# Kernel tuning notes

Measured on AMD Instinct MI355X. Metric: run time of the kernel, lower is better.

Reference implementation:

```python
import jax, jax.numpy as jnp
import numpy as np

NUM_NODE = 50000
NUM_EDGE = 1_600_000
NUM_REL = 512
DIM = 64


def setup_inputs() -> dict:
    key = jax.random.key(0)
    k1, k2, k3, k4, k5, k6 = jax.random.split(key, 6)
    inp = jax.random.normal(k1, (NUM_NODE, DIM), dtype=jnp.float32)
    boundary = jax.random.normal(k2, (NUM_NODE, DIM), dtype=jnp.float32)
    node_in = jax.random.randint(k3, (NUM_EDGE,), 0, NUM_NODE)
    node_out = jax.random.randint(k4, (NUM_EDGE,), 0, NUM_NODE)
    rel = jax.random.randint(k5, (NUM_EDGE,), 0, NUM_REL)
    edge_list = jnp.stack([node_in, node_out, rel], axis=1).astype(jnp.int32)
    edge_weight = jnp.ones((NUM_EDGE,), dtype=jnp.float32)
    relation_weight = jax.random.normal(k6, (NUM_REL, DIM), dtype=jnp.float32)
    W = jax.random.normal(jax.random.fold_in(key, 7), (DIM, DIM), dtype=jnp.float32) / np.sqrt(DIM)
    b = jnp.zeros((DIM,), dtype=jnp.float32)
    return {"input": inp, "boundary": boundary, "edge_list": edge_list,
            "edge_weight": edge_weight, "relation_weight": relation_weight,
            "W": W, "b": b}


def reference(input, boundary, edge_list, edge_weight, relation_weight, W, b):
    node_in = edge_list[:, 0]
    node_out = edge_list[:, 1]
    rel = edge_list[:, 2]
    # message: DistMult = x_src * r_e   [E, D]
    msg = input[node_in] * relation_weight[rel]
    msg = msg * edge_weight[:, None]
    # std aggregation: sum and sq_sum scatters, boundary acts as an extra self-message
    s = jax.ops.segment_sum(msg, node_out, num_segments=NUM_NODE) + boundary
    sq = jax.ops.segment_sum(msg * msg, node_out, num_segments=NUM_NODE) + boundary * boundary
    deg = jax.ops.segment_sum(jnp.ones_like(edge_weight), node_out, num_segments=NUM_NODE)
    deg1 = (deg + 1.0)[:, None]  # degree_out + 1 (boundary counted)
    update = jnp.sqrt(jnp.clip(sq / deg1 - (s / deg1) ** 2, 1e-6))
    # add_model: single Linear (MLP with num_mlp_layer=1, no trailing activation)
    return update @ W.T + b
```

## Files before the change

kernel.cpp:

```cpp
#include <hip/hip_runtime.h>
#include <hip/hip_bf16.h>
#include <hip/hip_fp16.h>

#define NN  50000
#define NE  1600000
#define DIM 64
#define NBK 391

#define OFF_FLAGS  0
#define OFF_BOFF   8
#define OFF_BCNTP  400
#define OFF_BCURP  8000
#define OFF_INP16  50800
#define OFF_RELW16 1650800
#define OFF_EIDX_H 1667184

#define CHUNK 4096
#define SBCAP 7936

typedef __bf16 bf16x8 __attribute__((ext_vector_type(8)));
typedef __bf16 bf16x4 __attribute__((ext_vector_type(4)));
typedef float  f32x4  __attribute__((ext_vector_type(4)));

__device__ __forceinline__ float loadF(const void* p, int i, int bf) {
  if (bf) return __bfloat162float(((const __hip_bfloat16*)p)[i]);
  return ((const float*)p)[i];
}

__device__ __forceinline__ float4 loadF4(const void* p, int i4, int bf) {
  if (bf) {
    ushort4 u = ((const ushort4*)p)[i4];
    float4 f;
    union { unsigned int ui; float fl; } c;
    c.ui = (unsigned int)u.x << 16; f.x = c.fl;
    c.ui = (unsigned int)u.y << 16; f.y = c.fl;
    c.ui = (unsigned int)u.z << 16; f.z = c.fl;
    c.ui = (unsigned int)u.w << 16; f.w = c.fl;
    return f;
  }
  return ((const float4*)p)[i4];
}

__device__ __forceinline__ float4 h4f(ushort4 u) {
  float4 f;
  f.x = __half2float(__ushort_as_half(u.x));
  f.y = __half2float(__ushort_as_half(u.y));
  f.z = __half2float(__ushort_as_half(u.z));
  f.w = __half2float(__ushort_as_half(u.w));
  return f;
}

__device__ __forceinline__ void accum(ushort4 ua, ushort4 ur,
                                      float4& s4, float4& q4) {
  float4 a = h4f(ua), r = h4f(ur);
  float tx = a.x * r.x, ty = a.y * r.y, tz = a.z * r.z, tw = a.w * r.w;
  s4.x += tx; q4.x = fmaf(tx, tx, q4.x);
  s4.y += ty; q4.y = fmaf(ty, ty, q4.y);
  s4.z += tz; q4.z = fmaf(tz, tz, q4.z);
  s4.w += tw; q4.w = fmaf(tw, tw, q4.w);
}

__global__ void k_detect(const void* input, const void* boundary,
                         const void* relw, const void* W, const void* ew,
                         int* flags, int* bcntp) {
  __shared__ int cnt;
  int t = threadIdx.x;
  const void* arrs[4] = {input, boundary, relw, W};
  for (int a = 0; a < 4; ++a) {
    if (t == 0) cnt = 0;
    __syncthreads();
    const unsigned short* u = (const unsigned short*)arrs[a];
    unsigned ex = (u[2 * t] >> 7) & 0xFF;
    if (ex >= 100 && ex <= 140) atomicAdd(&cnt, 1);
    __syncthreads();
    if (t == 0) flags[a] = (cnt >= 32) ? 1 : 0;
    __syncthreads();
  }
  if (t == 0) {
    flags[4] = (((const unsigned short*)ew)[0] == 0x3F80) ? 1 : 0;
    flags[5] = 1;
  }
  for (int i = t; i < NBK * 16; i += 64) bcntp[i] = 0;
}

__global__ __launch_bounds__(256) void k_stage(const void* __restrict__ in,
                                               const void* __restrict__ rw,
                                               unsigned short* __restrict__ inph,
                                               unsigned short* __restrict__ rwh,
                                               const int* __restrict__ flags) {
  if (flags[0] || flags[2]) return;
  int i = blockIdx.x * 256 + threadIdx.x;
  if (i < NN * 16) {
    float4 v = ((const float4*)in)[i];
    ushort4 h;
    h.x = __half_as_ushort(__float2half(v.x));
    h.y = __half_as_ushort(__float2half(v.y));
    h.z = __half_as_ushort(__float2half(v.z));
    h.w = __half_as_ushort(__float2half(v.w));
    ((ushort4*)inph)[i] = h;
  }
  if (i < 512 * 16) {
    float4 v = ((const float4*)rw)[i];
    ushort4 h;
    h.x = __half_as_ushort(__float2half(v.x));
    h.y = __half_as_ushort(__float2half(v.y));
    h.z = __half_as_ushort(__float2half(v.z));
    h.w = __half_as_ushort(__float2half(v.w));
    ((ushort4*)rwh)[i] = h;
  }
}

__global__ __launch_bounds__(256) void k_bhist(const int* __restrict__ el,
                                               const void* __restrict__ ew,
                                               int* __restrict__ bcntp,
                                               int* __restrict__ flags) {
  __shared__ int lc[NBK];
  int t = threadIdx.x;
  int bfE = flags[4];
  for (int i = t; i < NBK; i += 256) lc[i] = 0;
  __syncthreads();
  int c0 = blockIdx.x * 8192;
  int bad = 0;
  for (int i = t; i < 8192; i += 256) {
    int e = c0 + i;
    if (e < NE) {
      atomicAdd(&lc[el[e * 3 + 1] >> 7], 1);
      if (loadF(ew, e, bfE) != 1.0f) bad = 1;
    }
  }
  if (bad) flags[5] = 0;
  __syncthreads();
  for (int i = t; i < NBK; i += 256)
    if (lc[i]) atomicAdd(&bcntp[i * 16], lc[i]);
}

__global__ __launch_bounds__(256) void k_scanb(const int* __restrict__ bcntp,
                                               int* __restrict__ boff,
                                               int* __restrict__ bcurp) {
  __shared__ int sc[256];
  int t = threadIdx.x;
  int i0 = 2 * t, i1 = 2 * t + 1;
  int a = (i0 < NBK) ? bcntp[i0 * 16] : 0;
  int b = (i1 < NBK) ? bcntp[i1 * 16] : 0;
  sc[t] = a + b;
  __syncthreads();
  for (int off = 1; off < 256; off <<= 1) {
    int v = (t >= off) ? sc[t - off] : 0;
    __syncthreads();
    sc[t] += v;
    __syncthreads();
  }
  int excl = sc[t] - (a + b);
  if (i0 < 392) boff[i0] = excl;
  if (i1 < 392) boff[i1] = excl + a;
  if (i0 < NBK) bcurp[i0 * 16] = excl;
  if (i1 < NBK) bcurp[i1 * 16] = excl + a;
}

__global__ __launch_bounds__(256) void k_parta(
    const int* __restrict__ el, int* __restrict__ bcurp,
    int* __restrict__ eidx, const int* __restrict__ flags,
    const int* __restrict__ boff, int gb0, int gb1, int cap) {
  __shared__ int stage[CHUNK];
  __shared__ unsigned short sbk[CHUNK];
  __shared__ int lh[NBK], lbase[NBK], lh2[NBK], gbs[NBK];
  __shared__ int sc[256];
  __shared__ int total;
  int t = threadIdx.x;
  int nb = gb1 - gb0;
  int c0 = blockIdx.x * CHUNK;
  int ones = flags[5];
  int base0 = boff[gb0];
  for (int i = t; i < nb; i += 256) { lh[i] = 0; lh2[i] = 0; }
  __syncthreads();
  for (int i = t; i < CHUNK; i += 256) {
    int e = c0 + i;
    if (e < NE) {
      int b = (el[e * 3 + 1] >> 7) - gb0;
      if (b >= 0 && b < nb) atomicAdd(&lh[b], 1);
    }
  }
  __syncthreads();
  int a0 = (2 * t < nb) ? lh[2 * t] : 0;
  int a1 = (2 * t + 1 < nb) ? lh[2 * t + 1] : 0;
  sc[t] = a0 + a1;
  __syncthreads();
  for (int off = 1; off < 256; off <<= 1) {
    int v = (t >= off) ? sc[t - off] : 0;
    __syncthreads();
    sc[t] += v;
    __syncthreads();
  }
  int excl = sc[t] - (a0 + a1);
  if (2 * t < nb) {
    lbase[2 * t] = excl;
    if (a0 > 0) gbs[2 * t] = atomicAdd(&bcurp[(gb0 + 2 * t) * 16], a0);
  }
  if (2 * t + 1 < nb) {
    lbase[2 * t + 1] = excl + a0;
    if (a1 > 0) gbs[2 * t + 1] = atomicAdd(&bcurp[(gb0 + 2 * t + 1) * 16], a1);
  }
  if (t == 255) total = sc[255];
  __syncthreads();
  for (int i = t; i < CHUNK; i += 256) {
    int e = c0 + i;
    if (e < NE) {
      int nout = el[e * 3 + 1];
      int b = (nout >> 7) - gb0;
      if (b >= 0 && b < nb) {
        int r = atomicAdd(&lh2[b], 1);
        int slot = lbase[b] + r;
        int rec = ones ? (el[e * 3] | (el[e * 3 + 2] << 16) |
                          ((nout & 127) << 25))
                       : (e | ((nout & 127) << 25));
        stage[slot] = rec;
        sbk[slot] = (unsigned short)b;
      }
    }
  }
  __syncthreads();
  int tot = total;
  for (int i = t; i < tot; i += 256) {
    int b = sbk[i];
    int dst = gbs[b] + (i - lbase[b]) - base0;
    if (dst >= 0 && dst < cap) eidx[dst] = stage[i];
  }
}

__global__ __launch_bounds__(1024, 8) void k_node(
    const void* __restrict__ input, const void* __restrict__ boundary,
    const int* __restrict__ el, const void* __restrict__ ew,
    const void* __restrict__ relw, const void* __restrict__ W,
    const void* __restrict__ bv, const int* __restrict__ boff,
    const int* __restrict__ eidx, const int* __restrict__ flags,
    const unsigned short* __restrict__ inph,
    const unsigned short* __restrict__ rwh,
    void* __restrict__ out, int gb0, int hi, int cap) {
  __shared__ int ld[SBCAP];
  __shared__ int ld2[SBCAP];
  __shared__ int lstart[128], lend[128], lcnt[128];
  __bf16 (*updb)[72] = reinterpret_cast<__bf16(*)[72]>(ld);

  int bfI = flags[0], bfB = flags[1], bfR = flags[2], bfW = flags[3],
      bfE = flags[4], ones = flags[5];
  int t = threadIdx.x;
  int wv = t >> 6, ln = t & 63;
  int g = ln >> 4;
  int k = ln & 15;
  int q = ln >> 4;
  int B = gb0 + blockIdx.x;
  int n0 = B * 128;
  int base0 = boff[gb0];
  int rbase = boff[B], rend = boff[B + 1];
  int cnt = rend - rbase;
  int fast = (cnt <= SBCAP) && (rend - base0 <= cap);

  if (t < 128) lcnt[t] = 0;
  __syncthreads();
  if (fast) {
    for (int i = t; i < cnt; i += 1024) ld[i] = eidx[rbase - base0 + i];
    __syncthreads();
    for (int i = t; i < cnt; i += 1024)
      atomicAdd(&lcnt[(((unsigned)ld[i]) >> 25) & 127], 1);
  }
  __syncthreads();
  if (t < 128) lend[t] = lcnt[t];
  __syncthreads();
  for (int off = 1; off < 128; off <<= 1) {
    int v = 0;
    if (t < 128 && t >= off) v = lend[t - off];
    __syncthreads();
    if (t < 128) lend[t] += v;
    __syncthreads();
  }
  if (t < 128) { lstart[t] = lend[t] - lcnt[t]; lcnt[t] = 0; }
  __syncthreads();
  if (fast) {
    for (int i = t; i < cnt; i += 1024) {
      int rec = ld[i];
      int l = (((unsigned)rec) >> 25) & 127;
      int r = atomicAdd(&lcnt[l], 1);
      ld2[lstart[l] + r] = rec;
    }
  }
  __syncthreads();

  const ushort4* ih4 = (const ushort4*)inph;
  const ushort4* rh4 = (const ushort4*)rwh;
  int hot = (!bfI && !bfR && ones && inph != 0) ? 1 : 0;

  for (int rr = 0; rr < 8; ++rr) {
    int row = wv * 8 + rr;
    int n = n0 + row;
    if (n >= hi) {
      if (g == 0) *(bf16x4*)&updb[row][4 * k] =
          bf16x4{(__bf16)0.f, (__bf16)0.f, (__bf16)0.f, (__bf16)0.f};
      continue;
    }
    float4 s4 = {0.f,0.f,0.f,0.f}, q4 = {0.f,0.f,0.f,0.f};
    float degf = 0.f;
    if (fast) {
      int start = lstart[row], end = lend[row];
      degf = (float)(end - start);
      if (hot) {
        for (int base = start; base < end; base += 64) {
          int mm = end - base; if (mm > 64) mm = 64;
          int rec = 0;
          if (ln < mm) rec = ld2[base + ln];
          int jq = mm >> 2;
          int jmax = (mm + 3) >> 2;
          int j = 0;
          for (; j + 4 <= jq; j += 4) {
            int pk0 = __shfl(rec, j * 4 + g);
            int pk1 = __shfl(rec, j * 4 + 4 + g);
            int pk2 = __shfl(rec, j * 4 + 8 + g);
            int pk3 = __shfl(rec, j * 4 + 12 + g);
            ushort4 a0 = ih4[(pk0 & 0xFFFF) * 16 + k];
            ushort4 r0 = rh4[((pk0 >> 16) & 0x1FF) * 16 + k];
            ushort4 a1 = ih4[(pk1 & 0xFFFF) * 16 + k];
            ushort4 r1 = rh4[((pk1 >> 16) & 0x1FF) * 16 + k];
            ushort4 a2 = ih4[(pk2 & 0xFFFF) * 16 + k];
            ushort4 r2 = rh4[((pk2 >> 16) & 0x1FF) * 16 + k];
            ushort4 a3 = ih4[(pk3 & 0xFFFF) * 16 + k];
            ushort4 r3 = rh4[((pk3 >> 16) & 0x1FF) * 16 + k];
            accum(a0, r0, s4, q4);
            accum(a1, r1, s4, q4);
            accum(a2, r2, s4, q4);
            accum(a3, r3, s4, q4);
          }
          for (; j < jq; ++j) {
            int pk = __shfl(rec, j * 4 + g);
            ushort4 a = ih4[(pk & 0xFFFF) * 16 + k];
            ushort4 r = rh4[((pk >> 16) & 0x1FF) * 16 + k];
            accum(a, r, s4, q4);
          }
          for (; j < jmax; ++j) {
            int slot = j * 4 + g;
            int pk = __shfl(rec, slot & 63);
            float wsel = (slot < mm) ? 1.0f : 0.0f;
            ushort4 ua = ih4[(pk & 0xFFFF) * 16 + k];
            ushort4 ur = rh4[((pk >> 16) & 0x1FF) * 16 + k];
            float4 a = h4f(ua), r = h4f(ur);
            float tx = a.x*r.x, ty = a.y*r.y, tz = a.z*r.z, tw = a.w*r.w;
            s4.x = fmaf(wsel, tx, s4.x); q4.x = fmaf(wsel*tx, tx, q4.x);
            s4.y = fmaf(wsel, ty, s4.y); q4.y = fmaf(wsel*ty, ty, q4.y);
            s4.z = fmaf(wsel, tz, s4.z); q4.z = fmaf(wsel*tz, tz, q4.z);
            s4.w = fmaf(wsel, tw, s4.w); q4.w = fmaf(wsel*tw, tw, q4.w);
          }
        }
      } else {
        for (int base = start; base < end; base += 64) {
          int mm = end - base; if (mm > 64) mm = 64;
          int rec = 0; float wrec = 0.0f;
          if (ln < mm) {
            rec = ld2[base + ln] & 0x1FFFFFF;
            if (!ones) wrec = loadF(ew, rec, bfE);
          }
          int jmax = (mm + 3) >> 2;
          for (int j = 0; j < jmax; ++j) {
            int slot = j * 4 + g;
            int rj = __shfl(rec, slot);
            int nin, rl; float wj;
            if (ones) { nin = rj & 0xFFFF; rl = (rj >> 16) & 0x1FF; wj = 1.0f; }
            else      { nin = el[rj * 3]; rl = el[rj * 3 + 2];
                        wj = __shfl(wrec, slot); }
            float wsel = (slot < mm) ? wj : 0.0f;
            float4 a = loadF4(input, nin * 16 + k, bfI);
            float4 r = loadF4(relw, rl * 16 + k, bfR);
            float tx = a.x*r.x, ty = a.y*r.y, tz = a.z*r.z, tw = a.w*r.w;
            s4.x = fmaf(wsel, tx, s4.x); q4.x = fmaf(wsel*tx, tx, q4.x);
            s4.y = fmaf(wsel, ty, s4.y); q4.y = fmaf(wsel*ty, ty, q4.y);
            s4.z = fmaf(wsel, tz, s4.z); q4.z = fmaf(wsel*tz, tz, q4.z);
            s4.w = fmaf(wsel, tw, s4.w); q4.w = fmaf(wsel*tw, tw, q4.w);
          }
        }
      }
    } else {
      float degc = 0.f;
      for (int e0 = g; e0 < NE; e0 += 4) {
        int nout = el[e0 * 3 + 1];
        if (nout != n) continue;
        degc += 1.0f;
        int nin = el[e0 * 3], rl = el[e0 * 3 + 2];
        float wj = ones ? 1.0f : loadF(ew, e0, bfE);
        float4 a = loadF4(input, nin * 16 + k, bfI);
        float4 r = loadF4(relw, rl * 16 + k, bfR);
        float tx = wj*a.x*r.x, ty = wj*a.y*r.y, tz = wj*a.z*r.z,
              tw = wj*a.w*r.w;
        s4.x += tx; q4.x = fmaf(tx, tx, q4.x);
        s4.y += ty; q4.y = fmaf(ty, ty, q4.y);
        s4.z += tz; q4.z = fmaf(tz, tz, q4.z);
        s4.w += tw; q4.w = fmaf(tw, tw, q4.w);
      }
      degc += __shfl_xor(degc, 16); degc += __shfl_xor(degc, 32);
      degf = degc;
    }
    s4.x += __shfl_xor(s4.x, 16); s4.x += __shfl_xor(s4.x, 32);
    s4.y += __shfl_xor(s4.y, 16); s4.y += __shfl_xor(s4.y, 32);
    s4.z += __shfl_xor(s4.z, 16); s4.z += __shfl_xor(s4.z, 32);
    s4.w += __shfl_xor(s4.w, 16); s4.w += __shfl_xor(s4.w, 32);
    q4.x += __shfl_xor(q4.x, 16); q4.x += __shfl_xor(q4.x, 32);
    q4.y += __shfl_xor(q4.y, 16); q4.y += __shfl_xor(q4.y, 32);
    q4.z += __shfl_xor(q4.z, 16); q4.z += __shfl_xor(q4.z, 32);
    q4.w += __shfl_xor(q4.w, 16); q4.w += __shfl_xor(q4.w, 32);
    if (g == 0) {
      float4 b4 = loadF4(boundary, n * 16 + k, bfB);
      float dg = degf + 1.0f;
      float sv, qv;
      bf16x4 u;
      sv = (s4.x + b4.x) / dg; qv = (q4.x + b4.x * b4.x) / dg;
      u[0] = (__bf16)sqrtf(fmaxf(qv - sv * sv, 1e-6f));
      sv = (s4.y + b4.y) / dg; qv = (q4.y + b4.y * b4.y) / dg;
      u[1] = (__bf16)sqrtf(fmaxf(qv - sv * sv, 1e-6f));
      sv = (s4.z + b4.z) / dg; qv = (q4.z + b4.z * b4.z) / dg;
      u[2] = (__bf16)sqrtf(fmaxf(qv - sv * sv, 1e-6f));
      sv = (s4.w + b4.w) / dg; qv = (q4.w + b4.w * b4.w) / dg;
      u[3] = (__bf16)sqrtf(fmaxf(qv - sv * sv, 1e-6f));
      *(bf16x4*)&updb[row][4 * k] = u;
    }
  }
  __syncthreads();

  int tt = wv >> 1, chh = wv & 1;
  bf16x8 af0 = *(const bf16x8*)&updb[tt * 16 + (ln & 15)][q * 8];
  bf16x8 af1 = *(const bf16x8*)&updb[tt * 16 + (ln & 15)][32 + q * 8];
  #pragma unroll
  for (int hh = 0; hh < 2; ++hh) {
    int cc = chh * 32 + hh * 16 + (ln & 15);
    bf16x8 bfr0, bfr1;
    #pragma unroll
    for (int j = 0; j < 8; ++j) {
      bfr0[j] = (__bf16)loadF(W, cc * 64 + q * 8 + j, bfW);
      bfr1[j] = (__bf16)loadF(W, cc * 64 + 32 + q * 8 + j, bfW);
    }
    float bias = loadF(bv, cc, bfW);
    f32x4 accv = {0.f, 0.f, 0.f, 0.f};
    accv = __builtin_amdgcn_mfma_f32_16x16x32_bf16(af0, bfr0, accv, 0, 0, 0);
    accv = __builtin_amdgcn_mfma_f32_16x16x32_bf16(af1, bfr1, accv, 0, 0, 0);
    #pragma unroll
    for (int i = 0; i < 4; ++i) {
      int nn = n0 + tt * 16 + q * 4 + i;
      if (nn < hi) {
        float v = accv[i] + bias;
        if (bfI) ((__hip_bfloat16*)out)[nn * 64 + cc] = __float2bfloat16(v);
        else     ((float*)out)[nn * 64 + cc] = v;
      }
    }
  }
}

extern "C" void kernel_launch(void* const* d_in, const int* in_sizes, int n_in,
                              void* d_out, int out_size, void* d_ws, size_t ws_size,
                              hipStream_t stream) {
  const void* input    = d_in[0];
  const void* boundary = d_in[1];
  const int*  edges    = (const int*)d_in[2];
  const void* eweight  = d_in[3];
  const void* relw     = d_in[4];
  const void* W        = d_in[5];
  const void* bv       = d_in[6];

  int* wsI    = (int*)d_ws;
  int* flags  = wsI + OFF_FLAGS;
  int* boff   = wsI + OFF_BOFF;
  int* bcntp  = wsI + OFF_BCNTP;
  int* bcurp  = wsI + OFF_BCURP;

  long avail = (long)(ws_size / 4) - OFF_INP16;
  int useH = (avail >= (long)NE + 1600000 + 16384) ? 1 : 0;
  unsigned short* inph = useH ? (unsigned short*)(wsI + OFF_INP16) : 0;
  unsigned short* rwh  = useH ? (unsigned short*)(wsI + OFF_RELW16) : 0;
  int* eidx = useH ? (wsI + OFF_EIDX_H) : (wsI + OFF_INP16);
  long cap = useH ? (avail - 1600000 - 16384) : avail;
  if (cap < 1) cap = 1;
  int npass;
  if      (cap >= (long)NE) npass = 1;
  else if (cap >= 1000000)  npass = 2;
  else if (cap >= 520000)   npass = 4;
  else                      npass = 8;

  k_detect<<<1, 64, 0, stream>>>(input, boundary, relw, W, eweight,
                                 flags, bcntp);
  if (useH)
    k_stage<<<(NN * 16 + 255) / 256, 256, 0, stream>>>(input, relw, inph,
                                                       rwh, flags);
  k_bhist<<<(NE + 8191) / 8192, 256, 0, stream>>>(edges, eweight, bcntp,
                                                  flags);
  k_scanb<<<1, 256, 0, stream>>>(bcntp, boff, bcurp);

  const int PA_NB = (NE + CHUNK - 1) / CHUNK;
  for (int p = 0; p < npass; ++p) {
    int gb0 = NBK * p / npass;
    int gb1 = NBK * (p + 1) / npass;
    int hi = (gb1 * 128 < NN) ? gb1 * 128 : NN;
    k_parta<<<PA_NB, 256, 0, stream>>>(edges, bcurp, eidx, flags, boff,
                                       gb0, gb1, (int)cap);
    k_node<<<gb1 - gb0, 1024, 0, stream>>>(
        input, boundary, edges, eweight, relw, W, bv, boff, eidx, flags,
        inph, rwh, d_out, gb0, hi, (int)cap);
  }
}
```

Measured before the change: 239.0 us.

## Drop histogram/scan prepass and fp16 staging; use padded per-bucket edge slots

Removes the global bucket histogram and scan kernels by giving each 128-node bucket a fixed padded slot region (8192 entries) in the workspace. The partition kernel bumps per-bucket cursors directly, and the node kernel reads its count from those cursors. It also removes the fp16 staging copy of input and relation weights, so the node kernel gathers fp32 rows directly. This saves two launches and a full pass over the node features, but doubles the bytes per gather and uses more workspace. Buckets whose count exceeds the padded capacity drop to the slow path.

```diff
diff --git a/kernel.cpp b/kernel.cpp
--- a/kernel.cpp
+++ b/kernel.cpp
@@ -1,6 +1,5 @@
 #include <hip/hip_runtime.h>
 #include <hip/hip_bf16.h>
-#include <hip/hip_fp16.h>
 
 #define NN  50000
 #define NE  1600000
@@ -8,12 +7,8 @@
 #define NBK 391
 
 #define OFF_FLAGS  0
-#define OFF_BOFF   8
-#define OFF_BCNTP  400
-#define OFF_BCURP  8000
-#define OFF_INP16  50800
-#define OFF_RELW16 1650800
-#define OFF_EIDX_H 1667184
+#define OFF_BCURP  8
+#define OFF_EIDX   6272
 
 #define CHUNK 4096
 #define SBCAP 7936
@@ -41,18 +36,8 @@
   return ((const float4*)p)[i4];
 }
 
-__device__ __forceinline__ float4 h4f(ushort4 u) {
-  float4 f;
-  f.x = __half2float(__ushort_as_half(u.x));
-  f.y = __half2float(__ushort_as_half(u.y));
-  f.z = __half2float(__ushort_as_half(u.z));
-  f.w = __half2float(__ushort_as_half(u.w));
-  return f;
-}
-
-__device__ __forceinline__ void accum(ushort4 ua, ushort4 ur,
-                                      float4& s4, float4& q4) {
-  float4 a = h4f(ua), r = h4f(ur);
+__device__ __forceinline__ void accumF(float4 a, float4 r,
+                                       float4& s4, float4& q4) {
   float tx = a.x * r.x, ty = a.y * r.y, tz = a.z * r.z, tw = a.w * r.w;
   s4.x += tx; q4.x = fmaf(tx, tx, q4.x);
   s4.y += ty; q4.y = fmaf(ty, ty, q4.y);
@@ -62,7 +47,7 @@
 
 __global__ void k_detect(const void* input, const void* boundary,
                          const void* relw, const void* W, const void* ew,
-                         int* flags, int* bcntp) {
+                         int* flags, int* bcurp) {
   __shared__ int cnt;
   int t = threadIdx.x;
   const void* arrs[4] = {input, boundary, relw, W};
@@ -80,87 +65,25 @@
     flags[4] = (((const unsigned short*)ew)[0] == 0x3F80) ? 1 : 0;
     flags[5] = 1;
   }
-  for (int i = t; i < NBK * 16; i += 64) bcntp[i] = 0;
-}
-
-__global__ __launch_bounds__(256) void k_stage(const void* __restrict__ in,
-                                               const void* __restrict__ rw,
-                                               unsigned short* __restrict__ inph,
-                                               unsigned short* __restrict__ rwh,
-                                               const int* __restrict__ flags) {
-  if (flags[0] || flags[2]) return;
-  int i = blockIdx.x * 256 + threadIdx.x;
-  if (i < NN * 16) {
-    float4 v = ((const float4*)in)[i];
-    ushort4 h;
-    h.x = __half_as_ushort(__float2half(v.x));
-    h.y = __half_as_ushort(__float2half(v.y));
-    h.z = __half_as_ushort(__float2half(v.z));
-    h.w = __half_as_ushort(__float2half(v.w));
-    ((ushort4*)inph)[i] = h;
-  }
-  if (i < 512 * 16) {
-    float4 v = ((const float4*)rw)[i];
-    ushort4 h;
-    h.x = __half_as_ushort(__float2half(v.x));
-    h.y = __half_as_ushort(__float2half(v.y));
-    h.z = __half_as_ushort(__float2half(v.z));
-    h.w = __half_as_ushort(__float2half(v.w));
-    ((ushort4*)rwh)[i] = h;
-  }
-}
-
-__global__ __launch_bounds__(256) void k_bhist(const int* __restrict__ el,
-                                               const void* __restrict__ ew,
-                                               int* __restrict__ bcntp,
-                                               int* __restrict__ flags) {
-  __shared__ int lc[NBK];
-  int t = threadIdx.x;
+  for (int i = t; i < NBK * 16; i += 64) bcurp[i] = 0;
+}
+
+__global__ __launch_bounds__(256) void k_ew(const void* __restrict__ ew,
+                                            int* __restrict__ flags) {
   int bfE = flags[4];
-  for (int i = t; i < NBK; i += 256) lc[i] = 0;
-  __syncthreads();
   int c0 = blockIdx.x * 8192;
   int bad = 0;
-  for (int i = t; i < 8192; i += 256) {
+  for (int i = threadIdx.x; i < 8192; i += 256) {
     int e = c0 + i;
-    if (e < NE) {
-      atomicAdd(&lc[el[e * 3 + 1] >> 7], 1);
-      if (loadF(ew, e, bfE) != 1.0f) bad = 1;
-    }
+    if (e < NE && loadF(ew, e, bfE) != 1.0f) bad = 1;
   }
   if (bad) flags[5] = 0;
-  __syncthreads();
-  for (int i = t; i < NBK; i += 256)
-    if (lc[i]) atomicAdd(&bcntp[i * 16], lc[i]);
-}
-
-__global__ __launch_bounds__(256) void k_scanb(const int* __restrict__ bcntp,
-                                               int* __restrict__ boff,
-                                               int* __restrict__ bcurp) {
-  __shared__ int sc[256];
-  int t = threadIdx.x;
-  int i0 = 2 * t, i1 = 2 * t + 1;
-  int a = (i0 < NBK) ? bcntp[i0 * 16] : 0;
-  int b = (i1 < NBK) ? bcntp[i1 * 16] : 0;
-  sc[t] = a + b;
-  __syncthreads();
-  for (int off = 1; off < 256; off <<= 1) {
-    int v = (t >= off) ? sc[t - off] : 0;
-    __syncthreads();
-    sc[t] += v;
-    __syncthreads();
-  }
-  int excl = sc[t] - (a + b);
-  if (i0 < 392) boff[i0] = excl;
-  if (i1 < 392) boff[i1] = excl + a;
-  if (i0 < NBK) bcurp[i0 * 16] = excl;
-  if (i1 < NBK) bcurp[i1 * 16] = excl + a;
 }
 
 __global__ __launch_bounds__(256) void k_parta(
     const int* __restrict__ el, int* __restrict__ bcurp,
     int* __restrict__ eidx, const int* __restrict__ flags,
-    const int* __restrict__ boff, int gb0, int gb1, int cap) {
+    int gb0, int gb1, int padcap) {
   __shared__ int stage[CHUNK];
   __shared__ unsigned short sbk[CHUNK];
   __shared__ int lh[NBK], lbase[NBK], lh2[NBK], gbs[NBK];
@@ -170,7 +93,6 @@
   int nb = gb1 - gb0;
   int c0 = blockIdx.x * CHUNK;
   int ones = flags[5];
-  int base0 = boff[gb0];
   for (int i = t; i < nb; i += 256) { lh[i] = 0; lh2[i] = 0; }
   __syncthreads();
   for (int i = t; i < CHUNK; i += 256) {
@@ -222,8 +144,8 @@
   int tot = total;
   for (int i = t; i < tot; i += 256) {
     int b = sbk[i];
-    int dst = gbs[b] + (i - lbase[b]) - base0;
-    if (dst >= 0 && dst < cap) eidx[dst] = stage[i];
+    int slot = gbs[b] + (i - lbase[b]);
+    if (slot < padcap) eidx[(long)b * padcap + slot] = stage[i];
   }
 }
 
@@ -231,11 +153,9 @@
     const void* __restrict__ input, const void* __restrict__ boundary,
     const int* __restrict__ el, const void* __restrict__ ew,
     const void* __restrict__ relw, const void* __restrict__ W,
-    const void* __restrict__ bv, const int* __restrict__ boff,
+    const void* __restrict__ bv, const int* __restrict__ bcurp,
     const int* __restrict__ eidx, const int* __restrict__ flags,
-    const unsigned short* __restrict__ inph,
-    const unsigned short* __restrict__ rwh,
-    void* __restrict__ out, int gb0, int hi, int cap) {
+    void* __restrict__ out, int gb0, int hi, int padcap) {
   __shared__ int ld[SBCAP];
   __shared__ int ld2[SBCAP];
   __shared__ int lstart[128], lend[128], lcnt[128];
@@ -250,15 +170,14 @@
   int q = ln >> 4;
   int B = gb0 + blockIdx.x;
   int n0 = B * 128;
-  int base0 = boff[gb0];
-  int rbase = boff[B], rend = boff[B + 1];
-  int cnt = rend - rbase;
-  int fast = (cnt <= SBCAP) && (rend - base0 <= cap);
+  int cnt = bcurp[B * 16];
+  int fast = (cnt <= SBCAP) && (cnt <= padcap);
+  const int* myeidx = eidx + (long)blockIdx.x * padcap;
 
   if (t < 128) lcnt[t] = 0;
   __syncthreads();
   if (fast) {
-    for (int i = t; i < cnt; i += 1024) ld[i] = eidx[rbase - base0 + i];
+    for (int i = t; i < cnt; i += 1024) ld[i] = myeidx[i];
     __syncthreads();
     for (int i = t; i < cnt; i += 1024)
       atomicAdd(&lcnt[(((unsigned)ld[i]) >> 25) & 127], 1);
@@ -285,9 +204,9 @@
   }
   __syncthreads();
 
-  const ushort4* ih4 = (const ushort4*)inph;
-  const ushort4* rh4 = (const ushort4*)rwh;
-  int hot = (!bfI && !bfR && ones && inph != 0) ? 1 : 0;
+  const float4* inp4 = (const float4*)input;
+  const float4* rw4  = (const float4*)relw;
+  int hot = (!bfI && !bfR && ones) ? 1 : 0;
 
   for (int rr = 0; rr < 8; ++rr) {
     int row = wv * 8 + rr;
@@ -315,32 +234,31 @@
             int pk1 = __shfl(rec, j * 4 + 4 + g);
             int pk2 = __shfl(rec, j * 4 + 8 + g);
             int pk3 = __shfl(rec, j * 4 + 12 + g);
-            ushort4 a0 = ih4[(pk0 & 0xFFFF) * 16 + k];
-            ushort4 r0 = rh4[((pk0 >> 16) & 0x1FF) * 16 + k];
-            ushort4 a1 = ih4[(pk1 & 0xFFFF) * 16 + k];
-            ushort4 r1 = rh4[((pk1 >> 16) & 0x1FF) * 16 + k];
-            ushort4 a2 = ih4[(pk2 & 0xFFFF) * 16 + k];
-            ushort4 r2 = rh4[((pk2 >> 16) & 0x1FF) * 16 + k];
-            ushort4 a3 = ih4[(pk3 & 0xFFFF) * 16 + k];
-            ushort4 r3 = rh4[((pk3 >> 16) & 0x1FF) * 16 + k];
-            accum(a0, r0, s4, q4);
-            accum(a1, r1, s4, q4);
-            accum(a2, r2, s4, q4);
-            accum(a3, r3, s4, q4);
+            float4 a0 = inp4[(pk0 & 0xFFFF) * 16 + k];
+            float4 r0 = rw4[((pk0 >> 16) & 0x1FF) * 16 + k];
+            float4 a1 = inp4[(pk1 & 0xFFFF) * 16 + k];
+            float4 r1 = rw4[((pk1 >> 16) & 0x1FF) * 16 + k];
+            float4 a2 = inp4[(pk2 & 0xFFFF) * 16 + k];
+            float4 r2 = rw4[((pk2 >> 16) & 0x1FF) * 16 + k];
+            float4 a3 = inp4[(pk3 & 0xFFFF) * 16 + k];
+            float4 r3 = rw4[((pk3 >> 16) & 0x1FF) * 16 + k];
+            accumF(a0, r0, s4, q4);
+            accumF(a1, r1, s4, q4);
+            accumF(a2, r2, s4, q4);
+            accumF(a3, r3, s4, q4);
           }
           for (; j < jq; ++j) {
             int pk = __shfl(rec, j * 4 + g);
-            ushort4 a = ih4[(pk & 0xFFFF) * 16 + k];
-            ushort4 r = rh4[((pk >> 16) & 0x1FF) * 16 + k];
-            accum(a, r, s4, q4);
+            float4 a = inp4[(pk & 0xFFFF) * 16 + k];
+            float4 r = rw4[((pk >> 16) & 0x1FF) * 16 + k];
+            accumF(a, r, s4, q4);
           }
           for (; j < jmax; ++j) {
             int slot = j * 4 + g;
             int pk = __shfl(rec, slot & 63);
             float wsel = (slot < mm) ? 1.0f : 0.0f;
-            ushort4 ua = ih4[(pk & 0xFFFF) * 16 + k];
-            ushort4 ur = rh4[((pk >> 16) & 0x1FF) * 16 + k];
-            float4 a = h4f(ua), r = h4f(ur);
+            float4 a = inp4[(pk & 0xFFFF) * 16 + k];
+            float4 r = rw4[((pk >> 16) & 0x1FF) * 16 + k];
             float tx = a.x*r.x, ty = a.y*r.y, tz = a.z*r.z, tw = a.w*r.w;
             s4.x = fmaf(wsel, tx, s4.x); q4.x = fmaf(wsel*tx, tx, q4.x);
             s4.y = fmaf(wsel, ty, s4.y); q4.y = fmaf(wsel*ty, ty, q4.y);
@@ -462,41 +380,30 @@
 
   int* wsI    = (int*)d_ws;
   int* flags  = wsI + OFF_FLAGS;
-  int* boff   = wsI + OFF_BOFF;
-  int* bcntp  = wsI + OFF_BCNTP;
   int* bcurp  = wsI + OFF_BCURP;
-
-  long avail = (long)(ws_size / 4) - OFF_INP16;
-  int useH = (avail >= (long)NE + 1600000 + 16384) ? 1 : 0;
-  unsigned short* inph = useH ? (unsigned short*)(wsI + OFF_INP16) : 0;
-  unsigned short* rwh  = useH ? (unsigned short*)(wsI + OFF_RELW16) : 0;
-  int* eidx = useH ? (wsI + OFF_EIDX_H) : (wsI + OFF_INP16);
-  long cap = useH ? (avail - 1600000 - 16384) : avail;
-  if (cap < 1) cap = 1;
-  int npass;
-  if      (cap >= (long)NE) npass = 1;
-  else if (cap >= 1000000)  npass = 2;
-  else if (cap >= 520000)   npass = 4;
-  else                      npass = 8;
+  int* eidx   = wsI + OFF_EIDX;
+
+  long avail = (long)(ws_size / 4) - OFF_EIDX;
+  if (avail < 1) avail = 1;
+  int padcap = 8192;
+  long bfit = avail / padcap;
+  if (bfit < 1) { padcap = (int)avail; bfit = 1; }
+  if (bfit > NBK) bfit = NBK;
+  int npass = (int)((NBK + bfit - 1) / bfit);
 
   k_detect<<<1, 64, 0, stream>>>(input, boundary, relw, W, eweight,
-                                 flags, bcntp);
-  if (useH)
-    k_stage<<<(NN * 16 + 255) / 256, 256, 0, stream>>>(input, relw, inph,
-                                                       rwh, flags);
-  k_bhist<<<(NE + 8191) / 8192, 256, 0, stream>>>(edges, eweight, bcntp,
-                                                  flags);
-  k_scanb<<<1, 256, 0, stream>>>(bcntp, boff, bcurp);
+                                 flags, bcurp);
+  k_ew<<<(NE + 8191) / 8192, 256, 0, stream>>>(eweight, flags);
 
   const int PA_NB = (NE + CHUNK - 1) / CHUNK;
   for (int p = 0; p < npass; ++p) {
-    int gb0 = NBK * p / npass;
-    int gb1 = NBK * (p + 1) / npass;
+    int gb0 = (int)((long)NBK * p / npass);
+    int gb1 = (int)((long)NBK * (p + 1) / npass);
     int hi = (gb1 * 128 < NN) ? gb1 * 128 : NN;
-    k_parta<<<PA_NB, 256, 0, stream>>>(edges, bcurp, eidx, flags, boff,
-                                       gb0, gb1, (int)cap);
+    k_parta<<<PA_NB, 256, 0, stream>>>(edges, bcurp, eidx, flags,
+                                       gb0, gb1, padcap);
     k_node<<<gb1 - gb0, 1024, 0, stream>>>(
-        input, boundary, edges, eweight, relw, W, bv, boff, eidx, flags,
-        inph, rwh, d_out, gb0, hi, (int)cap);
-  }
-}
+        input, boundary, edges, eweight, relw, W, bv, bcurp, eidx, flags,
+        d_out, gb0, hi, padcap);
+  }
+}
```

Result: faster. 224.6 us (-6.0%).
